# Kernel optimization log

Measured on AMD Instinct MI355X. Metric: run time of the kernel, lower is better.

## Reference

```python
import jax, jax.numpy as jnp
import numpy as np

EPS_NORM = 1e-12   # eps added to std in channel norm
EPS_VAR = 1e-8     # eps added to clamped variance before sqrt


def channel_norm(x):
    # torch code normalizes each channel by mean/std over (batch, H, W);
    # torch.std default is unbiased (ddof=1).
    mean = jnp.mean(x, axis=(0, 2, 3), keepdims=True)
    std = jnp.std(x, axis=(0, 2, 3), keepdims=True, ddof=1)
    return (x - mean) / (std + EPS_NORM)


def conv1x1(x, w, b):
    # 1x1 conv == per-pixel linear: x [B,C,H,W], w [O,C], b [O]
    return jnp.einsum('bchw,oc->bohw', x, w) + b[None, :, None, None]


def setup_inputs() -> dict:
    key = jax.random.key(0)
    ks = jax.random.split(key, 10)
    B, Cv, Cqk, H, W = 4, 512, 512, 64, 64
    wscale = 1.0 / np.sqrt(Cqk)
    return {
        'F_c': jax.random.normal(ks[0], (B, Cv, H, W), jnp.float32),
        'F_s': jax.random.normal(ks[1], (B, Cv, H, W), jnp.float32),
        'F_c_previous': jax.random.normal(ks[2], (B, Cqk, H, W), jnp.float32),
        'F_s_previous': jax.random.normal(ks[3], (B, Cqk, H, W), jnp.float32),
        'Wf': jax.random.normal(ks[4], (Cqk, Cqk), jnp.float32) * wscale,
        'bf': jnp.zeros((Cqk,), jnp.float32),
        'Wg': jax.random.normal(ks[5], (Cqk, Cqk), jnp.float32) * wscale,
        'bg': jnp.zeros((Cqk,), jnp.float32),
        'Wh': jax.random.normal(ks[6], (Cv, Cv), jnp.float32) * wscale,
        'bh': jnp.zeros((Cv,), jnp.float32),
    }


def reference(F_c, F_s, F_c_previous, F_s_previous, Wf, bf, Wg, bg, Wh, bh):
    B = F_c.shape[0]
    Cv = F_s.shape[1]
    Cqk = F_c_previous.shape[1]

    Q = conv1x1(channel_norm(F_c_previous), Wf, bf).reshape(B, Cqk, -1)  # [B,Cqk,Nc]
    K = conv1x1(channel_norm(F_s_previous), Wg, bg).reshape(B, Cqk, -1)  # [B,Cqk,Ns]
    V = conv1x1(F_s, Wh, bh).reshape(B, Cv, -1)                          # [B,Cv,Ns]

    # A = softmax(Q^T K) over key positions: [B, Nc, Ns]
    A = jax.nn.softmax(jnp.einsum('bcn,bcm->bnm', Q, K), axis=-1)

    # Attention-weighted mean and variance of V: M,var [B,Cv,Nc]
    M = jnp.einsum('bvm,bnm->bvn', V, A)
    var = jnp.einsum('bvm,bnm->bvn', V * V, A) - M * M
    S = jnp.sqrt(jnp.clip(var, 0.0) + EPS_VAR)

    F_c_norm = channel_norm(F_c).reshape(B, Cv, -1)  # [B,Cv,Nc]
    return jnp.nan_to_num(S) * F_c_norm + M
```

## Files before the change

kernel.cpp:

```cpp
#include <hip/hip_runtime.h>
#include <math.h>


constexpr int B = 4;
constexpr int C = 512;
constexpr int N = 4096;
constexpr int NC = 2048;
constexpr int C2 = 2 * C;
constexpr int KS = 3 * C;
constexpr int HK = N / 2;
constexpr float EPSN = 1e-12f;
constexpr float EPSV = 1e-8f;

typedef __attribute__((ext_vector_type(4))) float f32x4;
typedef __attribute__((ext_vector_type(8))) short bf16x8;

static __device__ __forceinline__ unsigned short f2bf(float x) {
    union { float f; unsigned u; } c; c.f = x;
    unsigned r = c.u + 0x7FFFu + ((c.u >> 16) & 1u);
    return (unsigned short)(r >> 16);
}
static __device__ __forceinline__ float bf2f(unsigned short b) {
    union { unsigned u; float f; } c; c.u = ((unsigned)b) << 16;
    return c.f;
}

__global__ __launch_bounds__(256) void stats_kernel(
    const float* __restrict__ fcp, const float* __restrict__ fsp,
    const float* __restrict__ fc, float* __restrict__ stats)
{
    int c = blockIdx.x;
    int which = blockIdx.y;
    const float* src = (which == 0) ? fcp : ((which == 1) ? fsp : fc);
    float s = 0.f, s2 = 0.f;
    for (int b = 0; b < B; ++b) {
        const float4* p = reinterpret_cast<const float4*>(src + (size_t)(b * C + c) * N);
        for (int i = threadIdx.x; i < N / 4; i += 256) {
            float4 v = p[i];
            s  += v.x + v.y + v.z + v.w;
            s2 += v.x * v.x + v.y * v.y + v.z * v.z + v.w * v.w;
        }
    }
#pragma unroll
    for (int off = 32; off > 0; off >>= 1) {
        s  += __shfl_down(s, off);
        s2 += __shfl_down(s2, off);
    }
    __shared__ float w1[4], w2[4];
    if ((threadIdx.x & 63) == 0) { w1[threadIdx.x >> 6] = s; w2[threadIdx.x >> 6] = s2; }
    __syncthreads();
    if (threadIdx.x == 0) {
        float S  = w1[0] + w1[1] + w1[2] + w1[3];
        float S2 = w2[0] + w2[1] + w2[2] + w2[3];
        float n = (float)(B * N);
        float mean = S / n;
        float var = (S2 - S * S / n) / (n - 1.0f);
        var = fmaxf(var, 0.f);
        float inv = 1.0f / (sqrtf(var) + EPSN);
        stats[(which * C + c) * 2 + 0] = mean;
        stats[(which * C + c) * 2 + 1] = inv;
    }
}

__global__ __launch_bounds__(256) void eff_weights_split(
    const float* __restrict__ Wf, const float* __restrict__ bf_,
    const float* __restrict__ Wg, const float* __restrict__ bg_,
    const float* __restrict__ Wh, const float* __restrict__ bh_,
    const float* __restrict__ stats,
    unsigned short* __restrict__ Wsf, unsigned short* __restrict__ Wsg,
    unsigned short* __restrict__ Wsh,
    float* __restrict__ bpf, float* __restrict__ bpg, float* __restrict__ bph)
{
    int o = blockIdx.x;
    int which = blockIdx.y;
    const float* W    = (which == 0) ? Wf  : (which == 1) ? Wg  : Wh;
    const float* bias = (which == 0) ? bf_ : (which == 1) ? bg_ : bh_;
    unsigned short* Ws = (which == 0) ? Wsf : (which == 1) ? Wsg : Wsh;
    float* bp          = (which == 0) ? bpf : (which == 1) ? bpg : bph;
    float corr = 0.f;
    for (int c = threadIdx.x; c < C; c += 256) {
        float wp;
        if (which < 2) {
            const float* st = stats + which * C * 2;
            wp = W[o * C + c] * st[c * 2 + 1];
            corr += wp * st[c * 2 + 0];
        } else {
            wp = W[o * C + c];
        }
        unsigned short h = f2bf(wp);
        unsigned short l = f2bf(wp - bf2f(h));
        Ws[(size_t)o * C2 + c]     = h;
        Ws[(size_t)o * C2 + C + c] = l;
    }
#pragma unroll
    for (int off = 32; off > 0; off >>= 1) corr += __shfl_down(corr, off);
    __shared__ float wr[4];
    if ((threadIdx.x & 63) == 0) wr[threadIdx.x >> 6] = corr;
    __syncthreads();
    if (threadIdx.x == 0) bp[o] = bias[o] - (wr[0] + wr[1] + wr[2] + wr[3]);
}

__global__ __launch_bounds__(256) void in_split_all(
    const float* __restrict__ F0, const float* __restrict__ F1,
    const float* __restrict__ F2,
    unsigned short* __restrict__ X0, unsigned short* __restrict__ X1,
    unsigned short* __restrict__ X2)
{
    int z = blockIdx.z;
    const float* F = (z == 0) ? F0 : (z == 1) ? F1 : F2;
    unsigned short* Xs = (z == 0) ? X0 : (z == 1) ? X1 : X2;
    __shared__ float t[64][65];
    int n0 = blockIdx.x * 64, c0 = blockIdx.y * 64;
    int tx = threadIdx.x & 15, ty = threadIdx.x >> 4;
#pragma unroll
    for (int it = 0; it < 4; ++it) {
        int cl = ty + it * 16;
        float4 v = *reinterpret_cast<const float4*>(&F[(size_t)(c0 + cl) * N + n0 + tx * 4]);
        t[cl][tx * 4 + 0] = v.x; t[cl][tx * 4 + 1] = v.y;
        t[cl][tx * 4 + 2] = v.z; t[cl][tx * 4 + 3] = v.w;
    }
    __syncthreads();
#pragma unroll
    for (int it = 0; it < 4; ++it) {
        int nl = ty + it * 16;
        unsigned short h[4], l[4];
#pragma unroll
        for (int j = 0; j < 4; ++j) {
            float v = t[tx * 4 + j][nl];
            h[j] = f2bf(v);
            l[j] = f2bf(v - bf2f(h[j]));
        }
        size_t base = (size_t)(n0 + nl) * C2 + c0 + tx * 4;
        *reinterpret_cast<ushort4*>(&Xs[base])     = make_ushort4(h[0], h[1], h[2], h[3]);
        *reinterpret_cast<ushort4*>(&Xs[base + C]) = make_ushort4(l[0], l[1], l[2], l[3]);
    }
}

__global__ __launch_bounds__(256) void conv_all(
    const unsigned short* __restrict__ Wsf, const unsigned short* __restrict__ Wsg,
    const unsigned short* __restrict__ Wsh,
    const unsigned short* __restrict__ X0, const unsigned short* __restrict__ X1,
    const unsigned short* __restrict__ X2,
    const float* __restrict__ bpf, const float* __restrict__ bpg,
    const float* __restrict__ bph,
    unsigned short* __restrict__ Qs, unsigned short* __restrict__ Ks,
    unsigned short* __restrict__ Tb)
{
    int z = blockIdx.z;
    const unsigned short* Ws = (z == 0) ? Wsf : (z == 1) ? Wsg : Wsh;
    const unsigned short* Xs = (z == 0) ? X0  : (z == 1) ? X1  : X2;
    const float* bias        = (z == 0) ? bpf : (z == 1) ? bpg : bph;

    __shared__ unsigned short lA[128 * 32];
    __shared__ unsigned short lB[128 * 32];
    const int tid  = threadIdx.x;
    const int wave = tid >> 6, lane = tid & 63;
    const int o0 = blockIdx.y * 128;
    const int n0 = blockIdx.x * 128;
    const int wr = (wave >> 1) * 64, wc = (wave & 1) * 64;
    f32x4 acc[4][4] = {};
    const int r1 = tid >> 2, c1 = (tid & 3) * 8;
    const int r2 = r1 + 64;
    const int rowA = lane & 15;
    const int kk   = (lane >> 4) * 8;

    for (int k0 = 0; k0 < KS; k0 += 32) {
        int acol = (k0 < 1024) ? k0 : k0 - 1024;
        int bcol = (k0 < 512)  ? k0 : k0 - 512;
        __syncthreads();
        __builtin_amdgcn_global_load_lds(
            (const __attribute__((address_space(1))) void*)&Ws[(size_t)(o0 + r1) * C2 + acol + c1],
            (__attribute__((address_space(3))) void*)&lA[wave * 512], 16, 0, 0);
        __builtin_amdgcn_global_load_lds(
            (const __attribute__((address_space(1))) void*)&Ws[(size_t)(o0 + r2) * C2 + acol + c1],
            (__attribute__((address_space(3))) void*)&lA[2048 + wave * 512], 16, 0, 0);
        __builtin_amdgcn_global_load_lds(
            (const __attribute__((address_space(1))) void*)&Xs[(size_t)(n0 + r1) * C2 + bcol + c1],
            (__attribute__((address_space(3))) void*)&lB[wave * 512], 16, 0, 0);
        __builtin_amdgcn_global_load_lds(
            (const __attribute__((address_space(1))) void*)&Xs[(size_t)(n0 + r2) * C2 + bcol + c1],
            (__attribute__((address_space(3))) void*)&lB[2048 + wave * 512], 16, 0, 0);
        asm volatile("s_waitcnt vmcnt(0)" ::: "memory");
        __syncthreads();

        bf16x8 af[4], bfv[4];
#pragma unroll
        for (int f = 0; f < 4; ++f) {
            af[f]  = *reinterpret_cast<const bf16x8*>(&lA[(wr + f * 16 + rowA) * 32 + kk]);
            bfv[f] = *reinterpret_cast<const bf16x8*>(&lB[(wc + f * 16 + rowA) * 32 + kk]);
        }
#pragma unroll
        for (int fm = 0; fm < 4; ++fm)
#pragma unroll
            for (int fn = 0; fn < 4; ++fn)
                acc[fm][fn] = __builtin_amdgcn_mfma_f32_16x16x32_bf16(
                    af[fm], bfv[fn], acc[fm][fn], 0, 0, 0);
    }

    const int colD = lane & 15, rowD = (lane >> 4) * 4;
#pragma unroll
    for (int fm = 0; fm < 4; ++fm) {
        int ob = o0 + wr + fm * 16 + rowD;
        float4 b4 = *reinterpret_cast<const float4*>(&bias[ob]);
        float bv[4] = {b4.x, b4.y, b4.z, b4.w};
#pragma unroll
        for (int fn = 0; fn < 4; ++fn) {
            int n = n0 + wc + fn * 16 + colD;
            if (z < 2) {
                unsigned short* Yt = (z == 0) ? Qs : Ks;
                unsigned short hh[4], ll[4];
#pragma unroll
                for (int r = 0; r < 4; ++r) {
                    float val = acc[fm][fn][r] + bv[r];
                    hh[r] = f2bf(val);
                    ll[r] = f2bf(val - bf2f(hh[r]));
                }
                size_t base = (size_t)n * C2 + ob;
                *reinterpret_cast<ushort4*>(&Yt[base])     = make_ushort4(hh[0], hh[1], hh[2], hh[3]);
                *reinterpret_cast<ushort4*>(&Yt[base + C]) = make_ushort4(ll[0], ll[1], ll[2], ll[3]);
            } else {
#pragma unroll
                for (int r = 0; r < 4; ++r) {
                    float val = acc[fm][fn][r] + bv[r];
                    unsigned short vb = f2bf(val);
                    float vh = bf2f(vb);
                    float sq = vh * vh;
                    unsigned short qb = f2bf(sq);
                    unsigned short lb = f2bf(sq - bf2f(qb));
                    size_t rowb = (size_t)(ob + r) * N + n;
                    Tb[rowb]                     = vb;
                    Tb[rowb + (size_t)C * N]     = qb;
                    Tb[rowb + (size_t)2 * C * N] = lb;
                }
            }
        }
    }
}

__global__ __launch_bounds__(256) void gemm_qtk_mfma(
    const unsigned short* __restrict__ Qs,
    const unsigned short* __restrict__ Ks,
    float* __restrict__ L, int nbase)
{
    __shared__ unsigned short lA[128 * 32];
    __shared__ unsigned short lB[128 * 32];
    const int tid  = threadIdx.x;
    const int wave = tid >> 6, lane = tid & 63;
    const int nl0 = blockIdx.y * 128;
    const int qn0 = nbase + nl0;
    const int m0  = blockIdx.x * 128;
    const int wr = (wave >> 1) * 64, wc = (wave & 1) * 64;
    f32x4 acc[4][4] = {};
    const int r1 = tid >> 2, c1 = (tid & 3) * 8;
    const int r2 = r1 + 64;
    const int rowA = lane & 15;
    const int kk   = (lane >> 4) * 8;

    for (int k0 = 0; k0 < KS; k0 += 32) {
        int acol = (k0 < 1024) ? k0 : k0 - 1024;
        int bcol = (k0 < 512)  ? k0 : k0 - 512;
        __syncthreads();
        __builtin_amdgcn_global_load_lds(
            (const __attribute__((address_space(1))) void*)&Qs[(size_t)(qn0 + r1) * C2 + acol + c1],
            (__attribute__((address_space(3))) void*)&lA[wave * 512], 16, 0, 0);
        __builtin_amdgcn_global_load_lds(
            (const __attribute__((address_space(1))) void*)&Qs[(size_t)(qn0 + r2) * C2 + acol + c1],
            (__attribute__((address_space(3))) void*)&lA[2048 + wave * 512], 16, 0, 0);
        __builtin_amdgcn_global_load_lds(
            (const __attribute__((address_space(1))) void*)&Ks[(size_t)(m0 + r1) * C2 + bcol + c1],
            (__attribute__((address_space(3))) void*)&lB[wave * 512], 16, 0, 0);
        __builtin_amdgcn_global_load_lds(
            (const __attribute__((address_space(1))) void*)&Ks[(size_t)(m0 + r2) * C2 + bcol + c1],
            (__attribute__((address_space(3))) void*)&lB[2048 + wave * 512], 16, 0, 0);
        asm volatile("s_waitcnt vmcnt(0)" ::: "memory");
        __syncthreads();

        bf16x8 af[4], bfv[4];
#pragma unroll
        for (int f = 0; f < 4; ++f) {
            af[f]  = *reinterpret_cast<const bf16x8*>(&lA[(wr + f * 16 + rowA) * 32 + kk]);
            bfv[f] = *reinterpret_cast<const bf16x8*>(&lB[(wc + f * 16 + rowA) * 32 + kk]);
        }
#pragma unroll
        for (int fm = 0; fm < 4; ++fm)
#pragma unroll
            for (int fn = 0; fn < 4; ++fn)
                acc[fm][fn] = __builtin_amdgcn_mfma_f32_16x16x32_bf16(
                    af[fm], bfv[fn], acc[fm][fn], 0, 0, 0);
    }

    const int colD = lane & 15, rowD = (lane >> 4) * 4;
#pragma unroll
    for (int fm = 0; fm < 4; ++fm)
#pragma unroll
        for (int fn = 0; fn < 4; ++fn) {
            int col = m0 + wc + fn * 16 + colD;
            int row = nl0 + wr + fm * 16 + rowD;
#pragma unroll
            for (int r = 0; r < 4; ++r)
                L[(size_t)(row + r) * N + col] = acc[fm][fn][r];
        }
}

__global__ __launch_bounds__(256) void softmax_bf16(
    const float* __restrict__ L, unsigned short* __restrict__ E,
    float* __restrict__ rowinv)
{
    __shared__ float row[N];
    __shared__ float red[4];
    const float* Lr = L + (size_t)blockIdx.x * N;
    unsigned short* Er = E + (size_t)blockIdx.x * N;
    float mx = -3.0e38f;
    for (int i = threadIdx.x; i < N / 4; i += 256) {
        float4 v = reinterpret_cast<const float4*>(Lr)[i];
        reinterpret_cast<float4*>(row)[i] = v;
        mx = fmaxf(fmaxf(mx, fmaxf(v.x, v.y)), fmaxf(v.z, v.w));
    }
#pragma unroll
    for (int off = 32; off > 0; off >>= 1) mx = fmaxf(mx, __shfl_xor(mx, off));
    if ((threadIdx.x & 63) == 0) red[threadIdx.x >> 6] = mx;
    __syncthreads();
    mx = fmaxf(fmaxf(red[0], red[1]), fmaxf(red[2], red[3]));
    __syncthreads();
    float s = 0.f;
    for (int i = threadIdx.x; i < N / 4; i += 256) {
        float4 v = reinterpret_cast<float4*>(row)[i];
        unsigned short e0 = f2bf(__expf(v.x - mx));
        unsigned short e1 = f2bf(__expf(v.y - mx));
        unsigned short e2 = f2bf(__expf(v.z - mx));
        unsigned short e3 = f2bf(__expf(v.w - mx));
        s += bf2f(e0) + bf2f(e1) + bf2f(e2) + bf2f(e3);
        reinterpret_cast<ushort4*>(Er)[i] = make_ushort4(e0, e1, e2, e3);
    }
#pragma unroll
    for (int off = 32; off > 0; off >>= 1) s += __shfl_xor(s, off);
    if ((threadIdx.x & 63) == 0) red[threadIdx.x >> 6] = s;
    __syncthreads();
    if (threadIdx.x == 0)
        rowinv[blockIdx.x] = 1.0f / (red[0] + red[1] + red[2] + red[3]);
}

__global__ __launch_bounds__(256) void gemm_av_splitk(
    const unsigned short* __restrict__ T,
    const unsigned short* __restrict__ E,
    float* __restrict__ P)
{
    __shared__ unsigned short lA[128 * 32];
    __shared__ unsigned short lB[128 * 32];
    const int tid  = threadIdx.x;
    const int wave = tid >> 6, lane = tid & 63;
    const int v0 = blockIdx.y * 128;
    const int n0 = blockIdx.x * 128;
    const int kz = blockIdx.z;
    const int kbeg = kz * HK;
    const int wr = (wave >> 1) * 64, wc = (wave & 1) * 64;
    f32x4 acc[4][4] = {};
    const int r1 = tid >> 2, c1 = (tid & 3) * 8;
    const int r2 = r1 + 64;
    const int rowA = lane & 15;
    const int kk   = (lane >> 4) * 8;

    for (int k0 = kbeg; k0 < kbeg + HK; k0 += 32) {
        __syncthreads();
        __builtin_amdgcn_global_load_lds(
            (const __attribute__((address_space(1))) void*)&T[(size_t)(v0 + r1) * N + k0 + c1],
            (__attribute__((address_space(3))) void*)&lA[wave * 512], 16, 0, 0);
        __builtin_amdgcn_global_load_lds(
            (const __attribute__((address_space(1))) void*)&T[(size_t)(v0 + r2) * N + k0 + c1],
            (__attribute__((address_space(3))) void*)&lA[2048 + wave * 512], 16, 0, 0);
        __builtin_amdgcn_global_load_lds(
            (const __attribute__((address_space(1))) void*)&E[(size_t)(n0 + r1) * N + k0 + c1],
            (__attribute__((address_space(3))) void*)&lB[wave * 512], 16, 0, 0);
        __builtin_amdgcn_global_load_lds(
            (const __attribute__((address_space(1))) void*)&E[(size_t)(n0 + r2) * N + k0 + c1],
            (__attribute__((address_space(3))) void*)&lB[2048 + wave * 512], 16, 0, 0);
        asm volatile("s_waitcnt vmcnt(0)" ::: "memory");
        __syncthreads();

        bf16x8 af[4], bfv[4];
#pragma unroll
        for (int f = 0; f < 4; ++f) {
            af[f]  = *reinterpret_cast<const bf16x8*>(&lA[(wr + f * 16 + rowA) * 32 + kk]);
            bfv[f] = *reinterpret_cast<const bf16x8*>(&lB[(wc + f * 16 + rowA) * 32 + kk]);
        }
#pragma unroll
        for (int fm = 0; fm < 4; ++fm)
#pragma unroll
            for (int fn = 0; fn < 4; ++fn)
                acc[fm][fn] = __builtin_amdgcn_mfma_f32_16x16x32_bf16(
                    af[fm], bfv[fn], acc[fm][fn], 0, 0, 0);
    }

    float* Pz = P + (size_t)kz * 3 * C * NC;
    const int colD = lane & 15, rowD = (lane >> 4) * 4;
#pragma unroll
    for (int fm = 0; fm < 4; ++fm)
#pragma unroll
        for (int fn = 0; fn < 4; ++fn) {
            int col = n0 + wc + fn * 16 + colD;
            int row = v0 + wr + fm * 16 + rowD;
#pragma unroll
            for (int r = 0; r < 4; ++r)
                Pz[(size_t)(row + r) * NC + col] = acc[fm][fn][r];
        }
}

__global__ __launch_bounds__(256) void av_epilogue2(
    const float* __restrict__ P, const float* __restrict__ rowinv,
    const float* __restrict__ Fc, const float* __restrict__ st3,
    float* __restrict__ out, int nbase)
{
    const size_t PS = (size_t)3 * C * NC;
    int idx = blockIdx.x * 256 + threadIdx.x;
    int v = idx >> 9;
    int n = (idx & 511) * 4;
    float4 pm0 = *reinterpret_cast<const float4*>(&P[(size_t)v * NC + n]);
    float4 ph0 = *reinterpret_cast<const float4*>(&P[(size_t)(C + v) * NC + n]);
    float4 pl0 = *reinterpret_cast<const float4*>(&P[(size_t)(2 * C + v) * NC + n]);
    float4 pm1 = *reinterpret_cast<const float4*>(&P[PS + (size_t)v * NC + n]);
    float4 ph1 = *reinterpret_cast<const float4*>(&P[PS + (size_t)(C + v) * NC + n]);
    float4 pl1 = *reinterpret_cast<const float4*>(&P[PS + (size_t)(2 * C + v) * NC + n]);
    float4 ri = *reinterpret_cast<const float4*>(&rowinv[n]);
    float mean = st3[v * 2], inv = st3[v * 2 + 1];
    float4 fc = *reinterpret_cast<const float4*>(&Fc[(size_t)v * N + nbase + n]);
    float pmv[4] = {pm0.x + pm1.x, pm0.y + pm1.y, pm0.z + pm1.z, pm0.w + pm1.w};
    float phv[4] = {ph0.x + ph1.x + pl0.x + pl1.x, ph0.y + ph1.y + pl0.y + pl1.y,
                    ph0.z + ph1.z + pl0.z + pl1.z, ph0.w + ph1.w + pl0.w + pl1.w};
    float riv[4] = {ri.x, ri.y, ri.z, ri.w};
    float fcv[4] = {fc.x, fc.y, fc.z, fc.w};
    float o[4];
#pragma unroll
    for (int q = 0; q < 4; ++q) {
        float M  = pmv[q] * riv[q];
        float S2 = phv[q] * riv[q];
        float var = fmaxf(S2 - M * M, 0.f) + EPSV;
        o[q] = sqrtf(var) * ((fcv[q] - mean) * inv) + M;
    }
    *reinterpret_cast<float4*>(&out[(size_t)v * N + nbase + n]) =
        make_float4(o[0], o[1], o[2], o[3]);
}

extern "C" void kernel_launch(void* const* d_in, const int* in_sizes, int n_in,
                              void* d_out, int out_size, void* d_ws, size_t ws_size,
                              hipStream_t stream)
{
    const float* F_c      = (const float*)d_in[0];
    const float* F_s      = (const float*)d_in[1];
    const float* F_c_prev = (const float*)d_in[2];
    const float* F_s_prev = (const float*)d_in[3];
    const float* Wf = (const float*)d_in[4];
    const float* bf_ = (const float*)d_in[5];
    const float* Wg = (const float*)d_in[6];
    const float* bg_ = (const float*)d_in[7];
    const float* Wh = (const float*)d_in[8];
    const float* bh_ = (const float*)d_in[9];
    float* out = (float*)d_out;

    char* base = (char*)d_ws;
    size_t off = 0;
    auto alloc = [&](size_t bytes) { void* p = base + off; off = (off + bytes + 255) & ~(size_t)255; return p; };
    float* stats = (float*)alloc(3 * C * 2 * 4);
    float* bpf   = (float*)alloc(C * 4);
    float* bpg   = (float*)alloc(C * 4);
    float* bph   = (float*)alloc(C * 4);
    float* rinv  = (float*)alloc(NC * 4);
    unsigned short* Wsf = (unsigned short*)alloc((size_t)C * C2 * 2);
    unsigned short* Wsg = (unsigned short*)alloc((size_t)C * C2 * 2);
    unsigned short* Wsh = (unsigned short*)alloc((size_t)C * C2 * 2);
    unsigned short* Qs  = (unsigned short*)alloc((size_t)N * C2 * 2);
    unsigned short* Ks  = (unsigned short*)alloc((size_t)N * C2 * 2);
    unsigned short* Tb  = (unsigned short*)alloc((size_t)3 * C * N * 2);
    char* Lreg = (char*)alloc((size_t)NC * N * 4);
    float* Lb = (float*)Lreg;
    float* Pb = (float*)Lreg;
    unsigned short* Xs0 = (unsigned short*)Lreg;
    unsigned short* Xs1 = (unsigned short*)(Lreg + (size_t)N * C2 * 2);
    unsigned short* Xs2 = (unsigned short*)(Lreg + (size_t)2 * N * C2 * 2);
    unsigned short* Eb  = (unsigned short*)alloc((size_t)NC * N * 2);
    if (ws_size < off) return;

    hipLaunchKernelGGL(stats_kernel, dim3(C, 3), dim3(256), 0, stream,
                       F_c_prev, F_s_prev, F_c, stats);
    hipLaunchKernelGGL(eff_weights_split, dim3(C, 3), dim3(256), 0, stream,
                       Wf, bf_, Wg, bg_, Wh, bh_, stats, Wsf, Wsg, Wsh, bpf, bpg, bph);

    for (int b = 0; b < B; ++b) {
        const float* Xq = F_c_prev + (size_t)b * C * N;
        const float* Xk = F_s_prev + (size_t)b * C * N;
        const float* Xv = F_s      + (size_t)b * C * N;

        hipLaunchKernelGGL(in_split_all, dim3(N / 64, C / 64, 3), dim3(256), 0, stream,
                           Xq, Xk, Xv, Xs0, Xs1, Xs2);
        hipLaunchKernelGGL(conv_all, dim3(N / 128, C / 128, 3), dim3(256), 0, stream,
                           Wsf, Wsg, Wsh, Xs0, Xs1, Xs2, bpf, bpg, bph, Qs, Ks, Tb);

        for (int chunk = 0; chunk < N / NC; ++chunk) {
            int nbase = chunk * NC;
            hipLaunchKernelGGL(gemm_qtk_mfma, dim3(N / 128, NC / 128), dim3(256), 0, stream,
                               Qs, Ks, Lb, nbase);
            hipLaunchKernelGGL(softmax_bf16, dim3(NC), dim3(256), 0, stream, Lb, Eb, rinv);
            hipLaunchKernelGGL(gemm_av_splitk, dim3(NC / 128, 3 * C / 128, 2), dim3(256), 0, stream,
                               Tb, Eb, Pb);
            hipLaunchKernelGGL(av_epilogue2, dim3((C * NC / 4) / 256), dim3(256), 0, stream,
                               Pb, rinv, F_c + (size_t)b * C * N, stats + 2 * C * 2,
                               out + (size_t)b * C * N, nbase);
        }
    }
}
```

Baseline: 1.210 ms.

## Use 128x64 GEMM tiles with XCD swizzle and single full-N AV GEMM per batch

All three MFMA GEMMs move from 128x128 to 128x64 block tiles, and the block index is remapped so that consecutive workgroups land on the same XCD for L2 reuse. The two attention chunks now both write their softmax outputs: the second chunk's E buffer overlays the Q/K workspace once Q/K are no longer needed. A single non-split-K AV GEMM then covers all N columns, followed by one epilogue per batch. This removes the split-K partial buffers and halves the number of AV and epilogue launches, at the cost of fewer MFMAs per LDS load in the smaller tiles.

```diff
diff --git a/kernel.cpp b/kernel.cpp
--- a/kernel.cpp
+++ b/kernel.cpp
@@ -8,7 +8,6 @@
 constexpr int NC = 2048;
 constexpr int C2 = 2 * C;
 constexpr int KS = 3 * C;
-constexpr int HK = N / 2;
 constexpr float EPSN = 1e-12f;
 constexpr float EPSV = 1e-8f;
 
@@ -23,6 +22,14 @@
 static __device__ __forceinline__ float bf2f(unsigned short b) {
     union { unsigned u; float f; } c; c.u = ((unsigned)b) << 16;
     return c.f;
+}
+
+static __device__ __forceinline__ void xcd_swz(int gy, int& bx, int& by) {
+    int nwg = gy << 6;
+    int oldid = blockIdx.y * 64 + blockIdx.x;
+    int nid = (oldid & 7) * (nwg >> 3) + (oldid >> 3);
+    bx = nid & 63;
+    by = nid >> 6;
 }
 
 __global__ __launch_bounds__(256) void stats_kernel(
@@ -152,13 +159,14 @@
     const float* bias        = (z == 0) ? bpf : (z == 1) ? bpg : bph;
 
     __shared__ unsigned short lA[128 * 32];
-    __shared__ unsigned short lB[128 * 32];
+    __shared__ unsigned short lB[64 * 32];
     const int tid  = threadIdx.x;
     const int wave = tid >> 6, lane = tid & 63;
-    const int o0 = blockIdx.y * 128;
-    const int n0 = blockIdx.x * 128;
-    const int wr = (wave >> 1) * 64, wc = (wave & 1) * 64;
-    f32x4 acc[4][4] = {};
+    int bx, by; xcd_swz(4, bx, by);
+    const int o0 = by * 128;
+    const int n0 = bx * 64;
+    const int wr = (wave >> 1) * 64, wc = (wave & 1) * 32;
+    f32x4 acc[4][2] = {};
     const int r1 = tid >> 2, c1 = (tid & 3) * 8;
     const int r2 = r1 + 64;
     const int rowA = lane & 15;
@@ -177,22 +185,20 @@
         __builtin_amdgcn_global_load_lds(
             (const __attribute__((address_space(1))) void*)&Xs[(size_t)(n0 + r1) * C2 + bcol + c1],
             (__attribute__((address_space(3))) void*)&lB[wave * 512], 16, 0, 0);
-        __builtin_amdgcn_global_load_lds(
-            (const __attribute__((address_space(1))) void*)&Xs[(size_t)(n0 + r2) * C2 + bcol + c1],
-            (__attribute__((address_space(3))) void*)&lB[2048 + wave * 512], 16, 0, 0);
         asm volatile("s_waitcnt vmcnt(0)" ::: "memory");
         __syncthreads();
 
-        bf16x8 af[4], bfv[4];
-#pragma unroll
-        for (int f = 0; f < 4; ++f) {
+        bf16x8 af[4], bfv[2];
+#pragma unroll
+        for (int f = 0; f < 4; ++f)
             af[f]  = *reinterpret_cast<const bf16x8*>(&lA[(wr + f * 16 + rowA) * 32 + kk]);
+#pragma unroll
+        for (int f = 0; f < 2; ++f)
             bfv[f] = *reinterpret_cast<const bf16x8*>(&lB[(wc + f * 16 + rowA) * 32 + kk]);
-        }
 #pragma unroll
         for (int fm = 0; fm < 4; ++fm)
 #pragma unroll
-            for (int fn = 0; fn < 4; ++fn)
+            for (int fn = 0; fn < 2; ++fn)
                 acc[fm][fn] = __builtin_amdgcn_mfma_f32_16x16x32_bf16(
                     af[fm], bfv[fn], acc[fm][fn], 0, 0, 0);
     }
@@ -204,7 +210,7 @@
         float4 b4 = *reinterpret_cast<const float4*>(&bias[ob]);
         float bv[4] = {b4.x, b4.y, b4.z, b4.w};
 #pragma unroll
-        for (int fn = 0; fn < 4; ++fn) {
+        for (int fn = 0; fn < 2; ++fn) {
             int n = n0 + wc + fn * 16 + colD;
             if (z < 2) {
                 unsigned short* Yt = (z == 0) ? Qs : Ks;
@@ -243,14 +249,15 @@
     float* __restrict__ L, int nbase)
 {
     __shared__ unsigned short lA[128 * 32];
-    __shared__ unsigned short lB[128 * 32];
+    __shared__ unsigned short lB[64 * 32];
     const int tid  = threadIdx.x;
     const int wave = tid >> 6, lane = tid & 63;
-    const int nl0 = blockIdx.y * 128;
+    int bx, by; xcd_swz(16, bx, by);
+    const int nl0 = by * 128;
     const int qn0 = nbase + nl0;
-    const int m0  = blockIdx.x * 128;
-    const int wr = (wave >> 1) * 64, wc = (wave & 1) * 64;
-    f32x4 acc[4][4] = {};
+    const int m0  = bx * 64;
+    const int wr = (wave >> 1) * 64, wc = (wave & 1) * 32;
+    f32x4 acc[4][2] = {};
     const int r1 = tid >> 2, c1 = (tid & 3) * 8;
     const int r2 = r1 + 64;
     const int rowA = lane & 15;
@@ -269,22 +276,20 @@
         __builtin_amdgcn_global_load_lds(
             (const __attribute__((address_space(1))) void*)&Ks[(size_t)(m0 + r1) * C2 + bcol + c1],
             (__attribute__((address_space(3))) void*)&lB[wave * 512], 16, 0, 0);
-        __builtin_amdgcn_global_load_lds(
-            (const __attribute__((address_space(1))) void*)&Ks[(size_t)(m0 + r2) * C2 + bcol + c1],
-            (__attribute__((address_space(3))) void*)&lB[2048 + wave * 512], 16, 0, 0);
         asm volatile("s_waitcnt vmcnt(0)" ::: "memory");
         __syncthreads();
 
-        bf16x8 af[4], bfv[4];
-#pragma unroll
-        for (int f = 0; f < 4; ++f) {
+        bf16x8 af[4], bfv[2];
+#pragma unroll
+        for (int f = 0; f < 4; ++f)
             af[f]  = *reinterpret_cast<const bf16x8*>(&lA[(wr + f * 16 + rowA) * 32 + kk]);
+#pragma unroll
+        for (int f = 0; f < 2; ++f)
             bfv[f] = *reinterpret_cast<const bf16x8*>(&lB[(wc + f * 16 + rowA) * 32 + kk]);
-        }
 #pragma unroll
         for (int fm = 0; fm < 4; ++fm)
 #pragma unroll
-            for (int fn = 0; fn < 4; ++fn)
+            for (int fn = 0; fn < 2; ++fn)
                 acc[fm][fn] = __builtin_amdgcn_mfma_f32_16x16x32_bf16(
                     af[fm], bfv[fn], acc[fm][fn], 0, 0, 0);
     }
@@ -293,7 +298,7 @@
 #pragma unroll
     for (int fm = 0; fm < 4; ++fm)
 #pragma unroll
-        for (int fn = 0; fn < 4; ++fn) {
+        for (int fn = 0; fn < 2; ++fn) {
             int col = m0 + wc + fn * 16 + colD;
             int row = nl0 + wr + fm * 16 + rowD;
 #pragma unroll
@@ -304,7 +309,7 @@
 
 __global__ __launch_bounds__(256) void softmax_bf16(
     const float* __restrict__ L, unsigned short* __restrict__ E,
-    float* __restrict__ rowinv)
+    float* __restrict__ rinv, int nbase)
 {
     __shared__ float row[N];
     __shared__ float red[4];
@@ -337,30 +342,32 @@
     if ((threadIdx.x & 63) == 0) red[threadIdx.x >> 6] = s;
     __syncthreads();
     if (threadIdx.x == 0)
-        rowinv[blockIdx.x] = 1.0f / (red[0] + red[1] + red[2] + red[3]);
-}
-
-__global__ __launch_bounds__(256) void gemm_av_splitk(
+        rinv[nbase + blockIdx.x] = 1.0f / (red[0] + red[1] + red[2] + red[3]);
+}
+
+__global__ __launch_bounds__(256) void gemm_av_mfma(
     const unsigned short* __restrict__ T,
-    const unsigned short* __restrict__ E,
+    const unsigned short* __restrict__ E0,
+    const unsigned short* __restrict__ E1,
     float* __restrict__ P)
 {
     __shared__ unsigned short lA[128 * 32];
-    __shared__ unsigned short lB[128 * 32];
+    __shared__ unsigned short lB[64 * 32];
     const int tid  = threadIdx.x;
     const int wave = tid >> 6, lane = tid & 63;
-    const int v0 = blockIdx.y * 128;
-    const int n0 = blockIdx.x * 128;
-    const int kz = blockIdx.z;
-    const int kbeg = kz * HK;
-    const int wr = (wave >> 1) * 64, wc = (wave & 1) * 64;
-    f32x4 acc[4][4] = {};
+    int bx, by; xcd_swz(12, bx, by);
+    const int v0 = by * 128;
+    const int n0 = bx * 64;
+    const unsigned short* Ep = (n0 < NC) ? E0 + (size_t)n0 * N
+                                         : E1 + (size_t)(n0 - NC) * N;
+    const int wr = (wave >> 1) * 64, wc = (wave & 1) * 32;
+    f32x4 acc[4][2] = {};
     const int r1 = tid >> 2, c1 = (tid & 3) * 8;
     const int r2 = r1 + 64;
     const int rowA = lane & 15;
     const int kk   = (lane >> 4) * 8;
 
-    for (int k0 = kbeg; k0 < kbeg + HK; k0 += 32) {
+    for (int k0 = 0; k0 < N; k0 += 32) {
         __syncthreads();
         __builtin_amdgcn_global_load_lds(
             (const __attribute__((address_space(1))) void*)&T[(size_t)(v0 + r1) * N + k0 + c1],
@@ -369,63 +376,55 @@
             (const __attribute__((address_space(1))) void*)&T[(size_t)(v0 + r2) * N + k0 + c1],
             (__attribute__((address_space(3))) void*)&lA[2048 + wave * 512], 16, 0, 0);
         __builtin_amdgcn_global_load_lds(
-            (const __attribute__((address_space(1))) void*)&E[(size_t)(n0 + r1) * N + k0 + c1],
+            (const __attribute__((address_space(1))) void*)&Ep[(size_t)r1 * N + k0 + c1],
             (__attribute__((address_space(3))) void*)&lB[wave * 512], 16, 0, 0);
-        __builtin_amdgcn_global_load_lds(
-            (const __attribute__((address_space(1))) void*)&E[(size_t)(n0 + r2) * N + k0 + c1],
-            (__attribute__((address_space(3))) void*)&lB[2048 + wave * 512], 16, 0, 0);
         asm volatile("s_waitcnt vmcnt(0)" ::: "memory");
         __syncthreads();
 
-        bf16x8 af[4], bfv[4];
-#pragma unroll
-        for (int f = 0; f < 4; ++f) {
+        bf16x8 af[4], bfv[2];
+#pragma unroll
+        for (int f = 0; f < 4; ++f)
             af[f]  = *reinterpret_cast<const bf16x8*>(&lA[(wr + f * 16 + rowA) * 32 + kk]);
+#pragma unroll
+        for (int f = 0; f < 2; ++f)
             bfv[f] = *reinterpret_cast<const bf16x8*>(&lB[(wc + f * 16 + rowA) * 32 + kk]);
-        }
 #pragma unroll
         for (int fm = 0; fm < 4; ++fm)
 #pragma unroll
-            for (int fn = 0; fn < 4; ++fn)
+            for (int fn = 0; fn < 2; ++fn)
                 acc[fm][fn] = __builtin_amdgcn_mfma_f32_16x16x32_bf16(
                     af[fm], bfv[fn], acc[fm][fn], 0, 0, 0);
     }
 
-    float* Pz = P + (size_t)kz * 3 * C * NC;
     const int colD = lane & 15, rowD = (lane >> 4) * 4;
 #pragma unroll
     for (int fm = 0; fm < 4; ++fm)
 #pragma unroll
-        for (int fn = 0; fn < 4; ++fn) {
+        for (int fn = 0; fn < 2; ++fn) {
             int col = n0 + wc + fn * 16 + colD;
             int row = v0 + wr + fm * 16 + rowD;
 #pragma unroll
             for (int r = 0; r < 4; ++r)
-                Pz[(size_t)(row + r) * NC + col] = acc[fm][fn][r];
+                P[(size_t)(row + r) * N + col] = acc[fm][fn][r];
         }
 }
 
-__global__ __launch_bounds__(256) void av_epilogue2(
-    const float* __restrict__ P, const float* __restrict__ rowinv,
+__global__ __launch_bounds__(256) void av_epilogue(
+    const float* __restrict__ P, const float* __restrict__ rinv,
     const float* __restrict__ Fc, const float* __restrict__ st3,
-    float* __restrict__ out, int nbase)
-{
-    const size_t PS = (size_t)3 * C * NC;
+    float* __restrict__ out)
+{
     int idx = blockIdx.x * 256 + threadIdx.x;
-    int v = idx >> 9;
-    int n = (idx & 511) * 4;
-    float4 pm0 = *reinterpret_cast<const float4*>(&P[(size_t)v * NC + n]);
-    float4 ph0 = *reinterpret_cast<const float4*>(&P[(size_t)(C + v) * NC + n]);
-    float4 pl0 = *reinterpret_cast<const float4*>(&P[(size_t)(2 * C + v) * NC + n]);
-    float4 pm1 = *reinterpret_cast<const float4*>(&P[PS + (size_t)v * NC + n]);
-    float4 ph1 = *reinterpret_cast<const float4*>(&P[PS + (size_t)(C + v) * NC + n]);
-    float4 pl1 = *reinterpret_cast<const float4*>(&P[PS + (size_t)(2 * C + v) * NC + n]);
-    float4 ri = *reinterpret_cast<const float4*>(&rowinv[n]);
+    int v = idx >> 10;
+    int n = (idx & 1023) * 4;
+    float4 pm = *reinterpret_cast<const float4*>(&P[(size_t)v * N + n]);
+    float4 ph = *reinterpret_cast<const float4*>(&P[(size_t)(C + v) * N + n]);
+    float4 pl = *reinterpret_cast<const float4*>(&P[(size_t)(2 * C + v) * N + n]);
+    float4 ri = *reinterpret_cast<const float4*>(&rinv[n]);
     float mean = st3[v * 2], inv = st3[v * 2 + 1];
-    float4 fc = *reinterpret_cast<const float4*>(&Fc[(size_t)v * N + nbase + n]);
-    float pmv[4] = {pm0.x + pm1.x, pm0.y + pm1.y, pm0.z + pm1.z, pm0.w + pm1.w};
-    float phv[4] = {ph0.x + ph1.x + pl0.x + pl1.x, ph0.y + ph1.y + pl0.y + pl1.y,
-                    ph0.z + ph1.z + pl0.z + pl1.z, ph0.w + ph1.w + pl0.w + pl1.w};
+    float4 fc = *reinterpret_cast<const float4*>(&Fc[(size_t)v * N + n]);
+    float pmv[4] = {pm.x, pm.y, pm.z, pm.w};
+    float phv[4] = {ph.x + pl.x, ph.y + pl.y, ph.z + pl.z, ph.w + pl.w};
     float riv[4] = {ri.x, ri.y, ri.z, ri.w};
     float fcv[4] = {fc.x, fc.y, fc.z, fc.w};
     float o[4];
@@ -436,7 +435,7 @@
         float var = fmaxf(S2 - M * M, 0.f) + EPSV;
         o[q] = sqrtf(var) * ((fcv[q] - mean) * inv) + M;
     }
-    *reinterpret_cast<float4*>(&out[(size_t)v * N + nbase + n]) =
+    *reinterpret_cast<float4*>(&out[(size_t)v * N + n]) =
         make_float4(o[0], o[1], o[2], o[3]);
 }
 
@@ -463,20 +462,22 @@
     float* bpf   = (float*)alloc(C * 4);
     float* bpg   = (float*)alloc(C * 4);
     float* bph   = (float*)alloc(C * 4);
-    float* rinv  = (float*)alloc(NC * 4);
+    float* rinv  = (float*)alloc(N * 4);
     unsigned short* Wsf = (unsigned short*)alloc((size_t)C * C2 * 2);
     unsigned short* Wsg = (unsigned short*)alloc((size_t)C * C2 * 2);
     unsigned short* Wsh = (unsigned short*)alloc((size_t)C * C2 * 2);
-    unsigned short* Qs  = (unsigned short*)alloc((size_t)N * C2 * 2);
-    unsigned short* Ks  = (unsigned short*)alloc((size_t)N * C2 * 2);
-    unsigned short* Tb  = (unsigned short*)alloc((size_t)3 * C * N * 2);
-    char* Lreg = (char*)alloc((size_t)NC * N * 4);
-    float* Lb = (float*)Lreg;
-    float* Pb = (float*)Lreg;
-    unsigned short* Xs0 = (unsigned short*)Lreg;
-    unsigned short* Xs1 = (unsigned short*)(Lreg + (size_t)N * C2 * 2);
-    unsigned short* Xs2 = (unsigned short*)(Lreg + (size_t)2 * N * C2 * 2);
-    unsigned short* Eb  = (unsigned short*)alloc((size_t)NC * N * 2);
+    char* Areg = (char*)alloc((size_t)2 * N * C2 * 2);
+    unsigned short* Qs = (unsigned short*)Areg;
+    unsigned short* Ks = (unsigned short*)(Areg + (size_t)N * C2 * 2);
+    unsigned short* E1 = (unsigned short*)Areg;
+    char* Breg = (char*)alloc((size_t)NC * N * 4);
+    unsigned short* Xs0 = (unsigned short*)Breg;
+    unsigned short* Xs1 = (unsigned short*)(Breg + (size_t)N * C2 * 2);
+    unsigned short* Xs2 = (unsigned short*)(Breg + (size_t)2 * N * C2 * 2);
+    float* Lb = (float*)Breg;
+    float* Pb = (float*)Breg;
+    unsigned short* Tb = (unsigned short*)alloc((size_t)3 * C * N * 2);
+    unsigned short* E0 = (unsigned short*)alloc((size_t)NC * N * 2);
     if (ws_size < off) return;
 
     hipLaunchKernelGGL(stats_kernel, dim3(C, 3), dim3(256), 0, stream,
@@ -491,19 +492,19 @@
 
         hipLaunchKernelGGL(in_split_all, dim3(N / 64, C / 64, 3), dim3(256), 0, stream,
                            Xq, Xk, Xv, Xs0, Xs1, Xs2);
-        hipLaunchKernelGGL(conv_all, dim3(N / 128, C / 128, 3), dim3(256), 0, stream,
+        hipLaunchKernelGGL(conv_all, dim3(N / 64, C / 128, 3), dim3(256), 0, stream,
                            Wsf, Wsg, Wsh, Xs0, Xs1, Xs2, bpf, bpg, bph, Qs, Ks, Tb);
 
-        for (int chunk = 0; chunk < N / NC; ++chunk) {
-            int nbase = chunk * NC;
-            hipLaunchKernelGGL(gemm_qtk_mfma, dim3(N / 128, NC / 128), dim3(256), 0, stream,
-                               Qs, Ks, Lb, nbase);
-            hipLaunchKernelGGL(softmax_bf16, dim3(NC), dim3(256), 0, stream, Lb, Eb, rinv);
-            hipLaunchKernelGGL(gemm_av_splitk, dim3(NC / 128, 3 * C / 128, 2), dim3(256), 0, stream,
-                               Tb, Eb, Pb);
-            hipLaunchKernelGGL(av_epilogue2, dim3((C * NC / 4) / 256), dim3(256), 0, stream,
-                               Pb, rinv, F_c + (size_t)b * C * N, stats + 2 * C * 2,
-                               out + (size_t)b * C * N, nbase);
-        }
-    }
-}
+        hipLaunchKernelGGL(gemm_qtk_mfma, dim3(N / 64, NC / 128), dim3(256), 0, stream,
+                           Qs, Ks, Lb, 0);
+        hipLaunchKernelGGL(softmax_bf16, dim3(NC), dim3(256), 0, stream, Lb, E0, rinv, 0);
+        hipLaunchKernelGGL(gemm_qtk_mfma, dim3(N / 64, NC / 128), dim3(256), 0, stream,
+                           Qs, Ks, Lb, NC);
+        hipLaunchKernelGGL(softmax_bf16, dim3(NC), dim3(256), 0, stream, Lb, E1, rinv, NC);
+        hipLaunchKernelGGL(gemm_av_mfma, dim3(N / 64, 3 * C / 128), dim3(256), 0, stream,
+                           Tb, E0, E1, Pb);
+        hipLaunchKernelGGL(av_epilogue, dim3((C * N / 4) / 256), dim3(256), 0, stream,
+                           Pb, rinv, F_c + (size_t)b * C * N, stats + 2 * C * 2,
+                           out + (size_t)b * C * N);
+    }
+}
```

New measurement: 1.177 ms. 1.03x faster.
